# Kernel optimization log

Measured on AMD Instinct MI355X. Metric: run time of the kernel, lower is better.

Reference implementation:

```python
import jax, jax.numpy as jnp
import numpy as np

B, N, D, H, W = 2, 6, 120, 32, 88
C = 128
Z, HO, WO = 1, 128, 128  # bev_feat_shape
N_POINTS = 1_000_000


def setup_inputs() -> dict:
    key = jax.random.key(0)
    k1, k2, k3, k4, k5 = jax.random.split(key, 5)
    depth = jax.random.normal(k1, (B, N, D, H, W), dtype=jnp.float32)
    feat = jax.random.normal(k2, (B, N, C, H, W), dtype=jnp.float32)
    ranks_depth = jax.random.randint(k3, (N_POINTS,), 0, B * N * D * H * W, dtype=jnp.int32)
    ranks_feat = jax.random.randint(k4, (N_POINTS,), 0, B * N * H * W, dtype=jnp.int32)
    ranks_bev = jnp.sort(jax.random.randint(k5, (N_POINTS,), 0, B * Z * HO * WO, dtype=jnp.int32))
    # Derive intervals (consecutive runs of equal ranks_bev), as the CUDA op expects.
    rb = np.asarray(ranks_bev)
    starts = np.concatenate([[0], np.nonzero(np.diff(rb))[0] + 1]).astype(np.int32)
    lengths = np.diff(np.concatenate([starts, [rb.shape[0]]])).astype(np.int32)
    return {
        "depth": depth,
        "feat": feat,
        "ranks_depth": ranks_depth,
        "ranks_feat": ranks_feat,
        "ranks_bev": ranks_bev,
        "interval_starts": jnp.asarray(starts),
        "interval_lengths": jnp.asarray(lengths),
    }


def reference(depth, feat, ranks_depth, ranks_feat, ranks_bev, interval_starts, interval_lengths):
    b, n, c, h, w = feat.shape
    # feat laid out [b,n,c,h,w]; ranks_feat indexes (b,n,h,w) positions -> put c last.
    feat_flat = feat.transpose(0, 1, 3, 4, 2).reshape(-1, c)  # [b*n*h*w, c]
    depth_flat = depth.reshape(-1)                            # [b*n*d*h*w]
    # Gather depth scalar and feature row per point, multiply.
    prod = depth_flat[ranks_depth][:, None] * feat_flat[ranks_feat]  # [n_points, c]
    # Interval-based accumulation == segment-sum over sorted ranks_bev.
    num_cells = b * Z * HO * WO
    out = jax.ops.segment_sum(prod, ranks_bev, num_segments=num_cells)  # [b*z*h*w, c]
    out = out.reshape(b, Z, HO, WO, c).transpose(0, 4, 1, 2, 3)  # [b, c, z, h, w]
    return out
```

## Files before the change

### kernel.cpp

```cpp
#include <hip/hip_runtime.h>
#include <hip/hip_bf16.h>

#define HW_    2816
#define C_     128
#define BN_    12
#define SPAT_  16384
#define CELLS_ 32768
#define CPB_   128

#define TF_BX     88
#define TF_BY     4
#define TF_BLOCKS (TF_BX * TF_BY * BN_)
#define PG_BLOCKS 512
#define IV_BLOCKS 128

__device__ __forceinline__ unsigned int f2bf_rne(float x) {
    const unsigned int u = __float_as_uint(x);
    return (u + 0x7fffu + ((u >> 16) & 1u)) >> 16;
}

__global__ __launch_bounds__(256) void prep_k(
        const float* __restrict__ feat, __hip_bfloat16* __restrict__ featT,
        const float* __restrict__ depth, const int* __restrict__ rd,
        const int* __restrict__ rf, unsigned int* __restrict__ pair, int n_points,
        const int* __restrict__ istart, const int* __restrict__ ilen,
        const int* __restrict__ rb, int4* __restrict__ iv4,
        int* __restrict__ map, int n_intervals) {
    __shared__ float tile[32][33];
    const int bid = blockIdx.x;
    const int tid = threadIdx.x;

    if (bid < TF_BLOCKS) {
        const int bn  = bid / (TF_BX * TF_BY);
        const int r   = bid - bn * (TF_BX * TF_BY);
        const int c0  = (r / TF_BX) * 32;
        const int hw0 = (r - (r / TF_BX) * TF_BX) * 32;
        const int x = tid & 31, y = tid >> 5;
        const float* src = feat + ((size_t)bn * C_ + c0) * HW_ + hw0;
        #pragma unroll
        for (int yy = y; yy < 32; yy += 8)
            tile[yy][x] = src[(size_t)yy * HW_ + x];
        __syncthreads();
        __hip_bfloat16* dst = featT + ((size_t)bn * HW_ + hw0) * C_ + c0;
        #pragma unroll
        for (int yy = y; yy < 32; yy += 8)
            dst[(size_t)yy * C_ + x] = __float2bfloat16(tile[x][yy]);
    } else if (bid < TF_BLOCKS + PG_BLOCKS) {
        const int t = (bid - TF_BLOCKS) * 256 + tid;
        const int S = PG_BLOCKS * 256;
        int idx[8], rfv[8];
        float v[8];
        #pragma unroll
        for (int u = 0; u < 8; ++u) {
            const int ii = t + u * S;
            const int cl = ii < n_points ? ii : t;
            idx[u] = rd[cl];
            rfv[u] = rf[cl];
        }
        #pragma unroll
        for (int u = 0; u < 8; ++u) v[u] = depth[idx[u]];
        #pragma unroll
        for (int u = 0; u < 8; ++u) {
            const int ii = t + u * S;
            if (ii < n_points)
                pair[ii] = (f2bf_rne(v[u]) << 16) | (unsigned)rfv[u];
        }
    } else {
        const int ivl = (bid - TF_BLOCKS - PG_BLOCKS) * 256 + tid;
        if (ivl < n_intervals) {
            const int s = istart[ivl];
            const int c = rb[s];
            iv4[ivl] = make_int4(s, ilen[ivl], c, 0);
            map[c] = ivl;
            const int cnext = (ivl + 1 < n_intervals) ? rb[istart[ivl + 1]] : CELLS_;
            for (int cc = c + 1; cc < cnext; ++cc) map[cc] = -1;
            if (ivl == 0) for (int cc = 0; cc < c; ++cc) map[cc] = -1;
        }
    }
}

__global__ __launch_bounds__(512, 4) void bevpool_cells_k(
        const unsigned int* __restrict__ pair,
        const uint4* __restrict__ featT,
        const int4* __restrict__ iv4,
        const int* __restrict__ map,
        float* __restrict__ out) {
    __shared__ float lds[CPB_][36];
    const int q     = blockIdx.x & 3;
    const int cb    = blockIdx.x >> 2;
    const int cell0 = cb * CPB_;
    const int tid   = threadIdx.x;

    for (int i = tid; i < CPB_ * 36; i += 512) (&lds[0][0])[i] = 0.f;
    __syncthreads();

    const int w    = tid >> 6;
    const int lane = tid & 63;
    const int g    = lane >> 2;
    const int sl   = lane & 3;
    const int lc   = w * 16 + g;
    const size_t hoff = (size_t)(q * 4 + sl);

    const int m  = map[cell0 + lc];
    const int4 v = iv4[m < 0 ? 0 : m];

    if (m >= 0) {
        const int start = v.x;
        const int end   = v.x + v.y;
        float acc[8] = {0.f, 0.f, 0.f, 0.f, 0.f, 0.f, 0.f, 0.f};

        for (int i = start; i < end; i += 4) {
            int cl_[4];
            unsigned pr_[4];
            float d_[4];
            uint4 f_[4];
            #pragma unroll
            for (int u = 0; u < 4; ++u) {
                const int ii = i + u;
                cl_[u] = (ii < end) ? ii : i;
            }
            #pragma unroll
            for (int u = 0; u < 4; ++u) pr_[u] = pair[cl_[u]];
            #pragma unroll
            for (int u = 0; u < 4; ++u) d_[u] = __uint_as_float(pr_[u] & 0xffff0000u);
            #pragma unroll
            for (int u = 1; u < 4; ++u) d_[u] = (i + u < end) ? d_[u] : 0.f;
            #pragma unroll
            for (int u = 0; u < 4; ++u)
                f_[u] = featT[(size_t)(pr_[u] & 0xffffu) * 16 + hoff];
            #pragma unroll
            for (int u = 0; u < 4; ++u) {
                const float d = d_[u];
                acc[0] = fmaf(d, __uint_as_float(f_[u].x << 16),         acc[0]);
                acc[1] = fmaf(d, __uint_as_float(f_[u].x & 0xffff0000u), acc[1]);
                acc[2] = fmaf(d, __uint_as_float(f_[u].y << 16),         acc[2]);
                acc[3] = fmaf(d, __uint_as_float(f_[u].y & 0xffff0000u), acc[3]);
                acc[4] = fmaf(d, __uint_as_float(f_[u].z << 16),         acc[4]);
                acc[5] = fmaf(d, __uint_as_float(f_[u].z & 0xffff0000u), acc[5]);
                acc[6] = fmaf(d, __uint_as_float(f_[u].w << 16),         acc[6]);
                acc[7] = fmaf(d, __uint_as_float(f_[u].w & 0xffff0000u), acc[7]);
            }
        }
        #pragma unroll
        for (int c = 0; c < 8; ++c) lds[lc][sl * 8 + c] = acc[c];
    }
    __syncthreads();

    const int cl  = tid & 127;
    const int chb = tid >> 7;
    const int b   = cell0 >> 14;
    const int sp0 = cell0 & (SPAT_ - 1);
    float* obase = out + ((size_t)b * C_ + q * 32) * SPAT_ + sp0;
    #pragma unroll
    for (int it = 0; it < 8; ++it) {
        const int ch = chb + 4 * it;
        obase[(size_t)ch * SPAT_ + cl] = lds[cl][ch];
    }
}

__global__ __launch_bounds__(256) void bevpool_fallback_k(const float* __restrict__ depth,
                                                          const float* __restrict__ feat,
                                                          const int* __restrict__ rd_arr,
                                                          const int* __restrict__ rf_arr,
                                                          const int* __restrict__ rb,
                                                          const int* __restrict__ istart,
                                                          const int* __restrict__ ilen,
                                                          float* __restrict__ out,
                                                          int n_intervals) {
    const int wave = (int)((blockIdx.x * blockDim.x + threadIdx.x) >> 6);
    const int lane = threadIdx.x & 63;
    if (wave >= n_intervals) return;
    const int start = istart[wave];
    const int len   = ilen[wave];
    const int cell  = rb[start];
    float ax = 0.f, ay = 0.f;
    const int end = start + len;
    for (int i = start; i < end; ++i) {
        const int rfi = rf_arr[i];
        const int bn  = rfi / HW_;
        const int hw  = rfi - bn * HW_;
        const float d = depth[rd_arr[i]];
        const float* frow = feat + (size_t)bn * (C_ * HW_) + hw;
        ax = fmaf(d, frow[(size_t)(2 * lane)     * HW_], ax);
        ay = fmaf(d, frow[(size_t)(2 * lane + 1) * HW_], ay);
    }
    const int b  = cell >> 14;
    const int sp = cell & (SPAT_ - 1);
    float* o = out + (size_t)b * ((size_t)C_ * SPAT_) + sp;
    o[(size_t)(2 * lane)     * SPAT_] = ax;
    o[(size_t)(2 * lane + 1) * SPAT_] = ay;
}

extern "C" void kernel_launch(void* const* d_in, const int* in_sizes, int n_in,
                              void* d_out, int out_size, void* d_ws, size_t ws_size,
                              hipStream_t stream) {
    const float* depth  = (const float*)d_in[0];
    const float* feat   = (const float*)d_in[1];
    const int*   rd     = (const int*)d_in[2];
    const int*   rf     = (const int*)d_in[3];
    const int*   rb     = (const int*)d_in[4];
    const int*   istart = (const int*)d_in[5];
    const int*   ilen   = (const int*)d_in[6];
    float*       out    = (float*)d_out;
    const int n_intervals = in_sizes[5];
    const int n_points    = in_sizes[2];

    const size_t featT_bytes = (size_t)BN_ * HW_ * C_ * sizeof(__hip_bfloat16);
    const size_t pair_bytes  = ((size_t)n_points * sizeof(unsigned int) + 15) & ~(size_t)15;
    const size_t iv4_bytes   = (size_t)CELLS_ * sizeof(int4);
    const size_t map_bytes   = (size_t)CELLS_ * sizeof(int);

    if (ws_size >= featT_bytes + pair_bytes + iv4_bytes + map_bytes &&
        n_intervals <= CELLS_) {
        __hip_bfloat16* featT = (__hip_bfloat16*)d_ws;
        unsigned int*   pair  = (unsigned int*)((char*)d_ws + featT_bytes);
        int4*           iv4   = (int4*)((char*)d_ws + featT_bytes + pair_bytes);
        int*            map   = (int*)((char*)d_ws + featT_bytes + pair_bytes + iv4_bytes);

        const int prep_blocks = TF_BLOCKS + PG_BLOCKS + IV_BLOCKS;
        prep_k<<<prep_blocks, 256, 0, stream>>>(
            feat, featT, depth, rd, rf, pair, n_points,
            istart, ilen, rb, iv4, map, n_intervals);

        bevpool_cells_k<<<(CELLS_ / CPB_) * 4, 512, 0, stream>>>(
            pair, (const uint4*)featT, iv4, map, out);
    } else {
        hipMemsetAsync(out, 0, (size_t)out_size * sizeof(float), stream);
        const int blocks = (n_intervals + 3) / 4;
        bevpool_fallback_k<<<blocks, 256, 0, stream>>>(
            depth, feat, rd, rf, rb, istart, ilen, out, n_intervals);
    }
}
```

Measured before the change: 72.53 us.

## Split each cell's points across 16 lane groups with shuffle reduction, persistent blocks

Reworks the gather-accumulate kernel so each wavefront handles 8 cells in turn. The 16 lane groups stride through one cell's points and then combine their partial sums with cross-lane shuffles, where before one 4-lane group walked a whole cell serially. Blocks grow to 1024 threads and each processes two 128-cell ranges, launching 512 blocks instead of 1024. The aim is to shorten per-thread serial loops and balance uneven interval lengths, at the cost of shuffle reductions, wasted lanes on short intervals, and extra syncs.

Result: slower. 93.58 us (+29.0%).

```diff
diff --git a/kernel.cpp b/kernel.cpp
--- a/kernel.cpp
+++ b/kernel.cpp
@@ -7,6 +7,7 @@
 #define SPAT_  16384
 #define CELLS_ 32768
 #define CPB_   128
+#define QBLK_  512
 
 #define TF_BX     88
 #define TF_BY     4
@@ -79,82 +80,90 @@
     }
 }
 
-__global__ __launch_bounds__(512, 4) void bevpool_cells_k(
+__global__ __launch_bounds__(1024, 8) void bevpool_cells_k(
         const unsigned int* __restrict__ pair,
         const uint4* __restrict__ featT,
         const int4* __restrict__ iv4,
         const int* __restrict__ map,
         float* __restrict__ out) {
-    __shared__ float lds[CPB_][36];
-    const int q     = blockIdx.x & 3;
-    const int cb    = blockIdx.x >> 2;
-    const int cell0 = cb * CPB_;
-    const int tid   = threadIdx.x;
-
-    for (int i = tid; i < CPB_ * 36; i += 512) (&lds[0][0])[i] = 0.f;
-    __syncthreads();
-
+    __shared__ float lds[CPB_][33];
+    const int bid  = blockIdx.x;
+    const int q    = bid & 3;
+    const int tid  = threadIdx.x;
     const int w    = tid >> 6;
     const int lane = tid & 63;
     const int g    = lane >> 2;
     const int sl   = lane & 3;
-    const int lc   = w * 16 + g;
     const size_t hoff = (size_t)(q * 4 + sl);
 
-    const int m  = map[cell0 + lc];
-    const int4 v = iv4[m < 0 ? 0 : m];
-
-    if (m >= 0) {
-        const int start = v.x;
-        const int end   = v.x + v.y;
-        float acc[8] = {0.f, 0.f, 0.f, 0.f, 0.f, 0.f, 0.f, 0.f};
-
-        for (int i = start; i < end; i += 4) {
-            int cl_[4];
-            unsigned pr_[4];
-            float d_[4];
-            uint4 f_[4];
-            #pragma unroll
-            for (int u = 0; u < 4; ++u) {
-                const int ii = i + u;
-                cl_[u] = (ii < end) ? ii : i;
+    #pragma unroll
+    for (int rr = 0; rr < 2; ++rr) {
+        const int range = (bid >> 2) + rr * (QBLK_ / 4);
+        const int cell0 = range * CPB_;
+
+        for (int i = tid; i < CPB_ * 33; i += 1024) (&lds[0][0])[i] = 0.f;
+        __syncthreads();
+
+        for (int cc = 0; cc < 8; ++cc) {
+            const int lc = w * 8 + cc;
+            const int m  = map[cell0 + lc];
+            if (m < 0) continue;
+            const int4 v    = iv4[m];
+            const int start = v.x;
+            const int end   = v.x + v.y;
+
+            float acc[8] = {0.f, 0.f, 0.f, 0.f, 0.f, 0.f, 0.f, 0.f};
+            for (int i = start + g; i < end; i += 32) {
+                const int i1 = (i + 16 < end) ? i + 16 : i;
+                const unsigned p0 = pair[i];
+                const unsigned p1 = pair[i1];
+                const float d0 = __uint_as_float(p0 & 0xffff0000u);
+                float d1 = __uint_as_float(p1 & 0xffff0000u);
+                d1 = (i + 16 < end) ? d1 : 0.f;
+                const uint4 f0 = featT[(size_t)(p0 & 0xffffu) * 16 + hoff];
+                const uint4 f1 = featT[(size_t)(p1 & 0xffffu) * 16 + hoff];
+                acc[0] = fmaf(d0, __uint_as_float(f0.x << 16),         acc[0]);
+                acc[1] = fmaf(d0, __uint_as_float(f0.x & 0xffff0000u), acc[1]);
+                acc[2] = fmaf(d0, __uint_as_float(f0.y << 16),         acc[2]);
+                acc[3] = fmaf(d0, __uint_as_float(f0.y & 0xffff0000u), acc[3]);
+                acc[4] = fmaf(d0, __uint_as_float(f0.z << 16),         acc[4]);
+                acc[5] = fmaf(d0, __uint_as_float(f0.z & 0xffff0000u), acc[5]);
+                acc[6] = fmaf(d0, __uint_as_float(f0.w << 16),         acc[6]);
+                acc[7] = fmaf(d0, __uint_as_float(f0.w & 0xffff0000u), acc[7]);
+                acc[0] = fmaf(d1, __uint_as_float(f1.x << 16),         acc[0]);
+                acc[1] = fmaf(d1, __uint_as_float(f1.x & 0xffff0000u), acc[1]);
+                acc[2] = fmaf(d1, __uint_as_float(f1.y << 16),         acc[2]);
+                acc[3] = fmaf(d1, __uint_as_float(f1.y & 0xffff0000u), acc[3]);
+                acc[4] = fmaf(d1, __uint_as_float(f1.z << 16),         acc[4]);
+                acc[5] = fmaf(d1, __uint_as_float(f1.z & 0xffff0000u), acc[5]);
+                acc[6] = fmaf(d1, __uint_as_float(f1.w << 16),         acc[6]);
+                acc[7] = fmaf(d1, __uint_as_float(f1.w & 0xffff0000u), acc[7]);
             }
             #pragma unroll
-            for (int u = 0; u < 4; ++u) pr_[u] = pair[cl_[u]];
-            #pragma unroll
-            for (int u = 0; u < 4; ++u) d_[u] = __uint_as_float(pr_[u] & 0xffff0000u);
-            #pragma unroll
-            for (int u = 1; u < 4; ++u) d_[u] = (i + u < end) ? d_[u] : 0.f;
-            #pragma unroll
-            for (int u = 0; u < 4; ++u)
-                f_[u] = featT[(size_t)(pr_[u] & 0xffffu) * 16 + hoff];
-            #pragma unroll
-            for (int u = 0; u < 4; ++u) {
-                const float d = d_[u];
-                acc[0] = fmaf(d, __uint_as_float(f_[u].x << 16),         acc[0]);
-                acc[1] = fmaf(d, __uint_as_float(f_[u].x & 0xffff0000u), acc[1]);
-                acc[2] = fmaf(d, __uint_as_float(f_[u].y << 16),         acc[2]);
-                acc[3] = fmaf(d, __uint_as_float(f_[u].y & 0xffff0000u), acc[3]);
-                acc[4] = fmaf(d, __uint_as_float(f_[u].z << 16),         acc[4]);
-                acc[5] = fmaf(d, __uint_as_float(f_[u].z & 0xffff0000u), acc[5]);
-                acc[6] = fmaf(d, __uint_as_float(f_[u].w << 16),         acc[6]);
-                acc[7] = fmaf(d, __uint_as_float(f_[u].w & 0xffff0000u), acc[7]);
+            for (int c = 0; c < 8; ++c) {
+                acc[c] += __shfl_down(acc[c], 32);
+                acc[c] += __shfl_down(acc[c], 16);
+                acc[c] += __shfl_down(acc[c], 8);
+                acc[c] += __shfl_down(acc[c], 4);
             }
-        }
-        #pragma unroll
-        for (int c = 0; c < 8; ++c) lds[lc][sl * 8 + c] = acc[c];
-    }
-    __syncthreads();
-
-    const int cl  = tid & 127;
-    const int chb = tid >> 7;
-    const int b   = cell0 >> 14;
-    const int sp0 = cell0 & (SPAT_ - 1);
-    float* obase = out + ((size_t)b * C_ + q * 32) * SPAT_ + sp0;
-    #pragma unroll
-    for (int it = 0; it < 8; ++it) {
-        const int ch = chb + 4 * it;
-        obase[(size_t)ch * SPAT_ + cl] = lds[cl][ch];
+            if (g == 0) {
+                #pragma unroll
+                for (int c = 0; c < 8; ++c) lds[lc][sl * 8 + c] = acc[c];
+            }
+        }
+        __syncthreads();
+
+        const int cl  = tid & 127;
+        const int chg = tid >> 7;
+        const int b   = cell0 >> 14;
+        const int sp0 = cell0 & (SPAT_ - 1);
+        float* obase = out + ((size_t)b * C_ + q * 32) * SPAT_ + sp0;
+        #pragma unroll
+        for (int it = 0; it < 4; ++it) {
+            const int ch = chg + 8 * it;
+            obase[(size_t)ch * SPAT_ + cl] = lds[cl][ch];
+        }
+        __syncthreads();
     }
 }
 
@@ -222,7 +231,7 @@
             feat, featT, depth, rd, rf, pair, n_points,
             istart, ilen, rb, iv4, map, n_intervals);
 
-        bevpool_cells_k<<<(CELLS_ / CPB_) * 4, 512, 0, stream>>>(
+        bevpool_cells_k<<<QBLK_, 1024, 0, stream>>>(
             pair, (const uint4*)featT, iv4, map, out);
     } else {
         hipMemsetAsync(out, 0, (size_t)out_size * sizeof(float), stream);
```
